# Kernel tuning notes

Hardware: AMD Instinct MI355X
Metric: run time of the kernel (lower is better)

## Reference

```python
import jax, jax.numpy as jnp
import numpy as np

N_QUBITS = 6
N_LAYERS = 8
N_CLASSES = 4
BATCH = 262144
DIM = 2 ** N_QUBITS  # 64


def setup_inputs() -> dict:
    key = jax.random.key(0)
    k1, k2, k3, k4 = jax.random.split(key, 4)
    x = jax.random.normal(k1, (BATCH, DIM), dtype=jnp.float32)
    # TorchLayer default init for StronglyEntanglingLayers weights: U(0, 2*pi)
    weights = jax.random.uniform(k2, (N_LAYERS, N_QUBITS, 3), dtype=jnp.float32,
                                 minval=0.0, maxval=2.0 * np.pi)
    fc_w = jax.random.normal(k3, (N_CLASSES, N_QUBITS), dtype=jnp.float32) * 0.3
    fc_b = jax.random.normal(k4, (N_CLASSES,), dtype=jnp.float32) * 0.1
    return {"x": x, "weights": weights, "fc_w": fc_w, "fc_b": fc_b}


def _rot_mats(weights):
    # PennyLane Rot(phi, theta, omega) = RZ(omega) RY(theta) RZ(phi)
    phi, theta, omega = weights[..., 0], weights[..., 1], weights[..., 2]
    c = jnp.cos(theta / 2)
    s = jnp.sin(theta / 2)
    m00 = jnp.exp(-0.5j * (phi + omega)) * c
    m01 = -jnp.exp(0.5j * (phi - omega)) * s
    m10 = jnp.exp(-0.5j * (phi - omega)) * s
    m11 = jnp.exp(0.5j * (phi + omega)) * c
    # [L, n, 2, 2] complex64
    return jnp.stack([jnp.stack([m00, m01], -1), jnp.stack([m10, m11], -1)], -2).astype(jnp.complex64)


def _apply_1q(state, U, q):
    # state: [B, 2, 2, 2, 2, 2, 2]; apply 2x2 gate U on qubit axis q+1
    ax = q + 1
    s = jnp.moveaxis(state, ax, -1)
    s = jnp.einsum('ij,...j->...i', U, s)
    return jnp.moveaxis(s, -1, ax)


def _cnot(state, c, t):
    # flip target qubit t on the control==1 slice of qubit c
    axc = c + 1
    s0 = jax.lax.index_in_dim(state, 0, axis=axc, keepdims=False)
    s1 = jax.lax.index_in_dim(state, 1, axis=axc, keepdims=False)
    t_ax = t + 1 if t < c else t  # target axis after removing control axis
    s1 = jnp.flip(s1, axis=t_ax)
    return jnp.stack([s0, s1], axis=axc)


def _pauli_z_signs():
    # qubit 0 is the most significant bit of the basis-state index
    bits = (jnp.arange(DIM)[:, None] >> jnp.arange(N_QUBITS - 1, -1, -1)[None, :]) & 1
    return (1 - 2 * bits).astype(jnp.float32)  # [DIM, N_QUBITS]


def reference(x, weights, fc_w, fc_b):
    B = x.shape[0]
    # F.normalize(p=2) + AmplitudeEmbedding(normalize=True) -> single L2 normalize
    xn = x / jnp.maximum(jnp.linalg.norm(x, axis=1, keepdims=True), 1e-12)
    state = xn.astype(jnp.complex64).reshape((B,) + (2,) * N_QUBITS)
    U = _rot_mats(weights)  # [L, n, 2, 2]
    for l in range(N_LAYERS):
        for q in range(N_QUBITS):
            state = _apply_1q(state, U[l, q], q)
        r = (l % (N_QUBITS - 1)) + 1  # StronglyEntanglingLayers default ranges
        for q in range(N_QUBITS):
            state = _cnot(state, q, (q + r) % N_QUBITS)
    probs = (state.real ** 2 + state.imag ** 2).reshape(B, DIM)
    expvals = probs @ _pauli_z_signs()  # [B, n] <Z_i>
    return expvals @ fc_w.T + fc_b
```

## Files before the change

### kernel.cpp

```cpp
#include <hip/hip_runtime.h>

#define NQ 6
#define DIM 64
#define NL 8

#define KP  136
#define APT 72
#define ROWS 128
#define PSP 68

typedef __attribute__((ext_vector_type(8))) short short8v;
typedef __attribute__((ext_vector_type(4))) float floatx4;

__device__ inline unsigned short f2bf_rne(float f) {
    unsigned u = __float_as_uint(f);
    u += 0x7FFF + ((u >> 16) & 1);
    return (unsigned short)(u >> 16);
}

__global__ __launch_bounds__(64) void qnn_prep(
    const float* __restrict__ wts,
    const float* __restrict__ fc_w,
    void* __restrict__ ws)
{
    __shared__ float gc[48][4];
    const int n   = threadIdx.x;
    const int col = blockIdx.x;

    if (n < 48) {
        float phi = wts[n*3+0], th = wts[n*3+1], om = wts[n*3+2];
        float ch = cosf(0.5f*th), sh = sinf(0.5f*th);
        float p  = 0.5f*(phi+om), m  = 0.5f*(phi-om);
        gc[n][0] = cosf(p)*ch;
        gc[n][1] = sinf(p)*ch;
        gc[n][2] = cosf(m)*sh;
        gc[n][3] = sinf(m)*sh;
    }
    __syncthreads();

    float ar = (n == col) ? 1.0f : 0.0f;
    float ai = 0.0f;

    #pragma unroll
    for (int l = 0; l < NL; ++l) {
        #pragma unroll
        for (int q = 0; q < NQ; ++q) {
            const int g     = l*NQ + q;
            const int shift = 5 - q;
            const int mask  = 1 << shift;
            const int b     = (n >> shift) & 1;
            const float cpch = gc[g][0];
            const float spch = gc[g][1];
            const float cmsh = gc[g][2];
            const float smsh = gc[g][3];
            const float pr = __shfl_xor(ar, mask, 64);
            const float pi = __shfl_xor(ai, mask, 64);
            const float udr = cpch;
            const float udi = b ?  spch : -spch;
            const float uor = b ?  cmsh : -cmsh;
            const float uoi = -smsh;
            const float nr = udr*ar - udi*ai + uor*pr - uoi*pi;
            const float ni = udr*ai + udi*ar + uor*pi + uoi*pr;
            ar = nr; ai = ni;
        }
        const int r = (l % (NQ - 1)) + 1;
        #pragma unroll
        for (int q = 0; q < NQ; ++q) {
            const int t     = (q + r) % NQ;
            const int cmask = 1 << (5 - q);
            const int tmask = 1 << (5 - t);
            const float pr = __shfl_xor(ar, tmask, 64);
            const float pi = __shfl_xor(ai, tmask, 64);
            const bool ctrl = (n & cmask) != 0;
            ar = ctrl ? pr : ar;
            ai = ctrl ? pi : ai;
        }
    }

    unsigned short* Bs = (unsigned short*)ws;
    unsigned short hr = f2bf_rne(ar);
    float hrf = __uint_as_float((unsigned)hr << 16);
    unsigned short lr = f2bf_rne(ar - hrf);
    unsigned short hi = f2bf_rne(ai);
    float hif = __uint_as_float((unsigned)hi << 16);
    unsigned short li = f2bf_rne(ai - hif);
    Bs[n*KP + col]           = hr;
    Bs[n*KP + 64 + col]      = lr;
    Bs[(64+n)*KP + col]      = hi;
    Bs[(64+n)*KP + 64 + col] = li;

    if (col == 0) {
        float m0=0.f, m1=0.f, m2=0.f, m3=0.f;
        #pragma unroll
        for (int q = 0; q < NQ; ++q) {
            const float sgn = 1.0f - 2.0f*(float)((n >> (5-q)) & 1);
            m0 = fmaf(sgn, fc_w[0*NQ+q], m0);
            m1 = fmaf(sgn, fc_w[1*NQ+q], m1);
            m2 = fmaf(sgn, fc_w[2*NQ+q], m2);
            m3 = fmaf(sgn, fc_w[3*NQ+q], m3);
        }
        float* Mo = (float*)((char*)ws + 128*KP*2);
        Mo[n*4+0]=m0; Mo[n*4+1]=m1; Mo[n*4+2]=m2; Mo[n*4+3]=m3;
    }
}

__global__ __launch_bounds__(256) void qnn_main(
    const float* __restrict__ x,
    const float* __restrict__ fc_b,
    const void* __restrict__ wsv,
    float* __restrict__ out)
{
    __shared__ __align__(16) unsigned short Bs[128*KP];
    __shared__ __align__(16) unsigned short As[ROWS*APT];
    __shared__ float Ml[DIM*4];

    const int tid = threadIdx.x;
    const int s0  = blockIdx.x * ROWS;

    {
        const floatx4* bg = (const floatx4*)wsv;
        floatx4* bl = (floatx4*)Bs;
        #pragma unroll
        for (int i = 0; i < (128*KP*2/16 + 255)/256; ++i) {
            int idx = tid + i*256;
            if (idx < 128*KP*2/16) bl[idx] = bg[idx];
        }
        const float* Mg = (const float*)((const char*)wsv + 128*KP*2);
        Ml[tid] = Mg[tid];
    }

    {
        const float4* xg = (const float4*)(x + (size_t)s0 * DIM);
        unsigned* A32 = (unsigned*)As;
        #pragma unroll
        for (int i = 0; i < 8; ++i) {
            int f = tid + i*256;
            int s = f >> 4, q = f & 15;
            float4 v = xg[(s << 4) + q];
            unsigned short h0 = f2bf_rne(v.x), h1 = f2bf_rne(v.y);
            unsigned short h2 = f2bf_rne(v.z), h3 = f2bf_rne(v.w);
            int w0 = s*(APT/2) + q*2;
            A32[w0]   = ((unsigned)h1 << 16) | h0;
            A32[w0+1] = ((unsigned)h3 << 16) | h2;
        }
    }
    __syncthreads();

    const int lane = tid & 63;
    const int w    = tid >> 6;
    const int l15  = lane & 15;
    const int quad = lane >> 4;

    floatx4 acc[2][8];
    #pragma unroll
    for (int mt = 0; mt < 2; ++mt)
        #pragma unroll
        for (int nt = 0; nt < 8; ++nt)
            acc[mt][nt] = (floatx4){0.f, 0.f, 0.f, 0.f};

    #pragma unroll
    for (int kk = 0; kk < 4; ++kk) {
        const int ak = ((kk & 1) << 5) + quad*8;
        const int bk = (kk << 5) + quad*8;
        short8v a0 = *(const short8v*)&As[(w*32 +      l15)*APT + ak];
        short8v a1 = *(const short8v*)&As[(w*32 + 16 + l15)*APT + ak];
        #pragma unroll
        for (int nt = 0; nt < 8; ++nt) {
            short8v b = *(const short8v*)&Bs[(nt*16 + l15)*KP + bk];
            acc[0][nt] = __builtin_amdgcn_mfma_f32_16x16x32_bf16(a0, b, acc[0][nt], 0, 0, 0);
            acc[1][nt] = __builtin_amdgcn_mfma_f32_16x16x32_bf16(a1, b, acc[1][nt], 0, 0, 0);
        }
    }

    __syncthreads();
    float* Ps = (float*)Bs;
    #pragma unroll
    for (int mt = 0; mt < 2; ++mt)
        #pragma unroll
        for (int nt = 0; nt < 4; ++nt)
            #pragma unroll
            for (int r = 0; r < 4; ++r) {
                float re = acc[mt][nt][r];
                float im = acc[mt][nt + 4][r];
                int srow = w*32 + mt*16 + quad*4 + r;
                Ps[srow*PSP + nt*16 + l15] = fmaf(re, re, im*im);
            }
    __syncthreads();

    {
        const int sA = tid >> 2, c = tid & 3;
        const float bc = fc_b[c];
        float sum0 = 0.f, ss0 = 0.f, sum1 = 0.f, ss1 = 0.f;
        #pragma unroll
        for (int col = 0; col < DIM; ++col) {
            float m  = Ml[col*4 + c];
            float p0 = Ps[sA*PSP + col];
            float p1 = Ps[(sA + 64)*PSP + col];
            ss0 += p0; sum0 = fmaf(p0, m, sum0);
            ss1 += p1; sum1 = fmaf(p1, m, sum1);
        }
        out[(size_t)(s0 + sA)*4 + c]      = sum0/ss0 + bc;
        out[(size_t)(s0 + sA + 64)*4 + c] = sum1/ss1 + bc;
    }
}

extern "C" void kernel_launch(void* const* d_in, const int* in_sizes, int n_in,
                              void* d_out, int out_size, void* d_ws, size_t ws_size,
                              hipStream_t stream) {
    const float* x    = (const float*)d_in[0];
    const float* wts  = (const float*)d_in[1];
    const float* fc_w = (const float*)d_in[2];
    const float* fc_b = (const float*)d_in[3];
    float* out = (float*)d_out;

    const int batch = in_sizes[0] / DIM;

    qnn_prep<<<DIM, DIM, 0, stream>>>(wts, fc_w, d_ws);
    qnn_main<<<batch / ROWS, 256, 0, stream>>>(x, fc_b, d_ws, out);
}
```

Before: 113.7 us.

## Load A fragments directly into registers and fuse epilogue via wave shuffles

The x tile is now loaded straight from global memory into MFMA A-operand registers, replacing the LDS staging buffer. The probability/Pauli-Z/fc epilogue is computed in registers and reduced across lanes with xor shuffles, replacing the LDS round trip and the extra barriers. Launch bounds now request two blocks per CU. Together these cut LDS footprint and traffic and remove synchronisation, at the cost of less coalesced global loads (each lane reads 32-byte chunks from strided rows) and more register pressure and shuffle work.

```diff
diff --git a/kernel.cpp b/kernel.cpp
--- a/kernel.cpp
+++ b/kernel.cpp
@@ -5,17 +5,15 @@
 #define NL 8
 
 #define KP  136
-#define APT 72
 #define ROWS 128
-#define PSP 68
 
 typedef __attribute__((ext_vector_type(8))) short short8v;
 typedef __attribute__((ext_vector_type(4))) float floatx4;
 
-__device__ inline unsigned short f2bf_rne(float f) {
+__device__ inline short f2bf_rne(float f) {
     unsigned u = __float_as_uint(f);
     u += 0x7FFF + ((u >> 16) & 1);
-    return (unsigned short)(u >> 16);
+    return (short)(u >> 16);
 }
 
 __global__ __launch_bounds__(64) void qnn_prep(
@@ -78,12 +76,12 @@
     }
 
     unsigned short* Bs = (unsigned short*)ws;
-    unsigned short hr = f2bf_rne(ar);
+    unsigned short hr = (unsigned short)f2bf_rne(ar);
     float hrf = __uint_as_float((unsigned)hr << 16);
-    unsigned short lr = f2bf_rne(ar - hrf);
-    unsigned short hi = f2bf_rne(ai);
+    unsigned short lr = (unsigned short)f2bf_rne(ar - hrf);
+    unsigned short hi = (unsigned short)f2bf_rne(ai);
     float hif = __uint_as_float((unsigned)hi << 16);
-    unsigned short li = f2bf_rne(ai - hif);
+    unsigned short li = (unsigned short)f2bf_rne(ai - hif);
     Bs[n*KP + col]           = hr;
     Bs[n*KP + 64 + col]      = lr;
     Bs[(64+n)*KP + col]      = hi;
@@ -104,53 +102,53 @@
     }
 }
 
-__global__ __launch_bounds__(256) void qnn_main(
+__global__ __launch_bounds__(256, 2) void qnn_main(
     const float* __restrict__ x,
     const float* __restrict__ fc_b,
     const void* __restrict__ wsv,
     float* __restrict__ out)
 {
     __shared__ __align__(16) unsigned short Bs[128*KP];
-    __shared__ __align__(16) unsigned short As[ROWS*APT];
     __shared__ float Ml[DIM*4];
 
     const int tid = threadIdx.x;
     const int s0  = blockIdx.x * ROWS;
-
-    {
-        const floatx4* bg = (const floatx4*)wsv;
-        floatx4* bl = (floatx4*)Bs;
-        #pragma unroll
-        for (int i = 0; i < (128*KP*2/16 + 255)/256; ++i) {
-            int idx = tid + i*256;
-            if (idx < 128*KP*2/16) bl[idx] = bg[idx];
-        }
-        const float* Mg = (const float*)((const char*)wsv + 128*KP*2);
-        Ml[tid] = Mg[tid];
-    }
-
-    {
-        const float4* xg = (const float4*)(x + (size_t)s0 * DIM);
-        unsigned* A32 = (unsigned*)As;
-        #pragma unroll
-        for (int i = 0; i < 8; ++i) {
-            int f = tid + i*256;
-            int s = f >> 4, q = f & 15;
-            float4 v = xg[(s << 4) + q];
-            unsigned short h0 = f2bf_rne(v.x), h1 = f2bf_rne(v.y);
-            unsigned short h2 = f2bf_rne(v.z), h3 = f2bf_rne(v.w);
-            int w0 = s*(APT/2) + q*2;
-            A32[w0]   = ((unsigned)h1 << 16) | h0;
-            A32[w0+1] = ((unsigned)h3 << 16) | h2;
-        }
-    }
-    __syncthreads();
-
     const int lane = tid & 63;
     const int w    = tid >> 6;
     const int l15  = lane & 15;
     const int quad = lane >> 4;
 
+    {
+        const floatx4* bg = (const floatx4*)wsv;
+        floatx4* bl = (floatx4*)Bs;
+        #pragma unroll
+        for (int i = 0; i < 9; ++i) {
+            int idx = tid + i*256;
+            if (idx < 128*KP*2/16) bl[idx] = bg[idx];
+        }
+        const float* Mg = (const float*)((const char*)wsv + 128*KP*2);
+        Ml[tid] = Mg[tid];
+    }
+
+    short8v afr[2][2];
+    #pragma unroll
+    for (int mt = 0; mt < 2; ++mt) {
+        const size_t row = (size_t)(s0 + w*32 + mt*16 + l15);
+        const float* xp = x + row*DIM + quad*8;
+        #pragma unroll
+        for (int h = 0; h < 2; ++h) {
+            float4 u0 = *(const float4*)(xp + h*32);
+            float4 u1 = *(const float4*)(xp + h*32 + 4);
+            short8v a;
+            a[0]=f2bf_rne(u0.x); a[1]=f2bf_rne(u0.y);
+            a[2]=f2bf_rne(u0.z); a[3]=f2bf_rne(u0.w);
+            a[4]=f2bf_rne(u1.x); a[5]=f2bf_rne(u1.y);
+            a[6]=f2bf_rne(u1.z); a[7]=f2bf_rne(u1.w);
+            afr[mt][h] = a;
+        }
+    }
+    __syncthreads();
+
     floatx4 acc[2][8];
     #pragma unroll
     for (int mt = 0; mt < 2; ++mt)
@@ -160,48 +158,75 @@
 
     #pragma unroll
     for (int kk = 0; kk < 4; ++kk) {
-        const int ak = ((kk & 1) << 5) + quad*8;
+        const int h  = kk & 1;
         const int bk = (kk << 5) + quad*8;
-        short8v a0 = *(const short8v*)&As[(w*32 +      l15)*APT + ak];
-        short8v a1 = *(const short8v*)&As[(w*32 + 16 + l15)*APT + ak];
         #pragma unroll
         for (int nt = 0; nt < 8; ++nt) {
             short8v b = *(const short8v*)&Bs[(nt*16 + l15)*KP + bk];
-            acc[0][nt] = __builtin_amdgcn_mfma_f32_16x16x32_bf16(a0, b, acc[0][nt], 0, 0, 0);
-            acc[1][nt] = __builtin_amdgcn_mfma_f32_16x16x32_bf16(a1, b, acc[1][nt], 0, 0, 0);
-        }
-    }
-
-    __syncthreads();
-    float* Ps = (float*)Bs;
+            acc[0][nt] = __builtin_amdgcn_mfma_f32_16x16x32_bf16(afr[0][h], b, acc[0][nt], 0, 0, 0);
+            acc[1][nt] = __builtin_amdgcn_mfma_f32_16x16x32_bf16(afr[1][h], b, acc[1][nt], 0, 0, 0);
+        }
+    }
+
+    floatx4 Mv[4];
+    #pragma unroll
+    for (int nt = 0; nt < 4; ++nt)
+        Mv[nt] = *(const floatx4*)&Ml[(nt*16 + l15)*4];
+
+    float q[2][4][5];
+    #pragma unroll
+    for (int mt = 0; mt < 2; ++mt)
+        #pragma unroll
+        for (int r = 0; r < 4; ++r)
+            #pragma unroll
+            for (int c = 0; c < 5; ++c) q[mt][r][c] = 0.f;
+
     #pragma unroll
     for (int mt = 0; mt < 2; ++mt)
         #pragma unroll
         for (int nt = 0; nt < 4; ++nt)
             #pragma unroll
             for (int r = 0; r < 4; ++r) {
-                float re = acc[mt][nt][r];
-                float im = acc[mt][nt + 4][r];
-                int srow = w*32 + mt*16 + quad*4 + r;
-                Ps[srow*PSP + nt*16 + l15] = fmaf(re, re, im*im);
+                const float re = acc[mt][nt][r];
+                const float im = acc[mt][nt + 4][r];
+                const float p  = fmaf(re, re, im*im);
+                q[mt][r][0] = fmaf(p, Mv[nt][0], q[mt][r][0]);
+                q[mt][r][1] = fmaf(p, Mv[nt][1], q[mt][r][1]);
+                q[mt][r][2] = fmaf(p, Mv[nt][2], q[mt][r][2]);
+                q[mt][r][3] = fmaf(p, Mv[nt][3], q[mt][r][3]);
+                q[mt][r][4] += p;
             }
-    __syncthreads();
-
-    {
-        const int sA = tid >> 2, c = tid & 3;
-        const float bc = fc_b[c];
-        float sum0 = 0.f, ss0 = 0.f, sum1 = 0.f, ss1 = 0.f;
-        #pragma unroll
-        for (int col = 0; col < DIM; ++col) {
-            float m  = Ml[col*4 + c];
-            float p0 = Ps[sA*PSP + col];
-            float p1 = Ps[(sA + 64)*PSP + col];
-            ss0 += p0; sum0 = fmaf(p0, m, sum0);
-            ss1 += p1; sum1 = fmaf(p1, m, sum1);
-        }
-        out[(size_t)(s0 + sA)*4 + c]      = sum0/ss0 + bc;
-        out[(size_t)(s0 + sA + 64)*4 + c] = sum1/ss1 + bc;
-    }
+
+    #pragma unroll
+    for (int mt = 0; mt < 2; ++mt)
+        #pragma unroll
+        for (int r = 0; r < 4; ++r)
+            #pragma unroll
+            for (int c = 0; c < 5; ++c) {
+                float v = q[mt][r][c];
+                v += __shfl_xor(v, 1, 64);
+                v += __shfl_xor(v, 2, 64);
+                v += __shfl_xor(v, 4, 64);
+                v += __shfl_xor(v, 8, 64);
+                q[mt][r][c] = v;
+            }
+
+    const float b0 = fc_b[0], b1 = fc_b[1], b2 = fc_b[2], b3 = fc_b[3];
+    #pragma unroll
+    for (int mt = 0; mt < 2; ++mt)
+        #pragma unroll
+        for (int r = 0; r < 4; ++r) {
+            const float inv = 1.0f / q[mt][r][4];
+            float4 o;
+            o.x = fmaf(q[mt][r][0], inv, b0);
+            o.y = fmaf(q[mt][r][1], inv, b1);
+            o.z = fmaf(q[mt][r][2], inv, b2);
+            o.w = fmaf(q[mt][r][3], inv, b3);
+            if (l15 == mt*4 + r) {
+                const int srow = w*32 + mt*16 + quad*4 + r;
+                *(float4*)(out + (size_t)(s0 + srow)*4) = o;
+            }
+        }
 }
 
 extern "C" void kernel_launch(void* const* d_in, const int* in_sizes, int n_in,
```

After: 116.3 us. 2.3% more time.
